# Kernel tuning notes

Hardware: AMD Instinct MI355X
Metric: run time of the kernel (lower is better)

Reference implementation:

```python
import jax, jax.numpy as jnp
import numpy as np

N, C, T, H, W = 16, 64, 30, 64, 44
PC = 64
OUT_H, OUT_W = 16, 20
T_RATE, H_RATE, W_RATE = 0.4, 4.0 / 8, 10.0 / 11  # torso
HEAD_H_RATE = 1.0 / 8
EPS = 1e-8


def setup_inputs() -> dict:
    key = jax.random.key(0)
    ks = jax.random.split(key, 8)
    x = jax.random.normal(ks[0], (N, C, T, H, W), jnp.float32)
    param_x = jax.random.normal(ks[1], (N, PC), jnp.float32)
    W1 = jax.random.normal(ks[2], (PC, PC // 2), jnp.float32) * 0.1
    b1 = jnp.zeros((PC // 2,), jnp.float32)
    W2 = jax.random.normal(ks[3], (PC // 2, 7), jnp.float32) * 0.1
    b2 = jnp.zeros((7,), jnp.float32)
    Wf = jax.random.normal(ks[4], (C, C), jnp.float32) * 0.05
    bf = jnp.zeros((C,), jnp.float32)
    return {"x": x, "param_x": param_x, "W1": W1, "b1": b1, "W2": W2, "b2": b2, "Wf": Wf, "bf": bf}


def reference(x, param_x, W1, b1, W2, b2, Wf, bf):
    n, c, t, h, w = x.shape
    dtype = x.dtype
    atten_in_t = t * T_RATE
    atten_in_h = h * H_RATE
    atten_in_w = w * W_RATE
    atten_ratio = atten_in_w / atten_in_h
    aout_h = int(round(OUT_W / atten_ratio))
    anchor_t = int(round(t / 2.0))
    anchor_x = int(round(w / 2.0))
    anchor_y = int(round(atten_in_h / 2.0 + h * HEAD_H_RATE))  # torso anchor

    # --- localization MLP (locator stand-in): param_x -> 7 params per sample ---
    hid = jnp.tanh(param_x @ W1 + b1)
    p = hid @ W2 + b2  # [N, 7]
    dt0, dx0, dy0 = p[:, 0:1], p[:, 1:2], p[:, 2:3]
    log_sigma2, log_delta_t, log_delta, log_gamma = p[:, 3:4], p[:, 4:5], p[:, 5:6], p[:, 6:7]

    dx = jnp.tanh(dx0) * atten_in_w / 2.0 + anchor_x          # [N,1]
    dy = jnp.tanh(dy0) * atten_in_h / 2.0 + anchor_y          # [N,1]
    sigma2 = jnp.exp(log_sigma2)                              # [N,1]
    delta = jnp.exp(log_delta) * W_RATE                      # [N,1]
    gamma = jax.nn.sigmoid(log_gamma)                         # [N,1]

    # --- spatial Gaussian filter banks ---
    gx = jnp.arange(OUT_W, dtype=dtype)
    gy = jnp.arange(aout_h, dtype=dtype)
    mu_x = dx + (gx - OUT_W / 2.0) * delta                    # [N, OUT_W]
    mu_y = dy + (gy - aout_h / 2.0) * delta                   # [N, aout_h]
    a = jnp.arange(w, dtype=dtype)
    b = jnp.arange(h, dtype=dtype)
    s2 = sigma2[:, :, None]                                   # [N,1,1]
    Fx = jnp.exp(-((a - mu_x[:, :, None]) ** 2) / (2.0 * s2))  # [N, OUT_W, W]
    Fy = jnp.exp(-((b - mu_y[:, :, None]) ** 2) / (2.0 * s2))  # [N, aout_h, H]
    Fx = Fx / jnp.maximum(jnp.sum(Fx, -1, keepdims=True), EPS)
    Fy = Fy / jnp.maximum(jnp.sum(Fy, -1, keepdims=True), EPS)

    # --- spatial sampling: Fy @ x @ Fx^T over the (C*T)-folded batch dim ---
    x2 = x.reshape(n, c * t, h, w)
    t1 = jnp.einsum('ndhw,nqw->ndhq', x2, Fx)                 # [N, C*T, H, OUT_W]
    g = jnp.einsum('nph,ndhq->ndpq', Fy, t1)                  # [N, C*T, aout_h, OUT_W]
    pad_t = (OUT_H - aout_h) // 2
    pad_b = OUT_H - pad_t - aout_h
    g = jnp.pad(g, ((0, 0), (0, 0), (pad_t, pad_b), (0, 0)))  # [N, C*T, OUT_H, OUT_W]

    # --- temporal linear resampling (grid_sample, align_corners=True, zero pad) ---
    dt = jnp.tanh(dt0) * atten_in_t / 2.0 + anchor_t          # [N,1]
    delta_t = jnp.exp(log_delta_t) * T_RATE                   # [N,1]
    gt = jnp.arange(t, dtype=dtype)
    mu_t = dt + (gt - t / 2.0) * delta_t                      # [N, T] raw frame positions

    gseq = g.reshape(n, c, t, OUT_H * OUT_W).transpose(0, 1, 3, 2).reshape(n, c * OUT_H * OUT_W, t)
    i0f = jnp.floor(mu_t)
    frac = mu_t - i0f
    i0 = i0f.astype(jnp.int32)
    i1 = i0 + 1

    def gather(idx):
        return jnp.take_along_axis(gseq, jnp.clip(idx, 0, t - 1)[:, None, :], axis=2)

    w0 = jnp.where((i0 >= 0) & (i0 < t), 1.0 - frac, 0.0)[:, None, :]
    w1 = jnp.where((i1 >= 0) & (i1 < t), frac, 0.0)[:, None, :]
    samp = gather(i0) * w0 + gather(i1) * w1                  # [N, C*OUT_H*OUT_W, T]
    out = samp.reshape(n, c, OUT_H, OUT_W, t).transpose(0, 1, 4, 2, 3)  # [N,C,T,OUT_H,OUT_W]

    out = out * gamma.reshape(n, 1, 1, 1, 1)
    # feature extraction: pointwise Conv3d (extractor stand-in)
    out = jnp.einsum('ncthw,oc->nothw', out, Wf) + bf[None, :, None, None, None]

    params = jnp.stack([dt[:, 0], dx[:, 0], dy[:, 0], sigma2[:, 0],
                        delta[:, 0], delta_t[:, 0], gamma[:, 0]], 0)  # [7, N]
    return out, jax.lax.stop_gradient(params)
```

## Files before the change

kernel.cpp:

```cpp
#include <hip/hip_runtime.h>
#include <math.h>

#define NN 16
#define CC 64
#define TT 30
#define HH 64
#define WW 44
#define OUTH 16
#define OUTW 20
#define HW 320

#define FX_OFF    0
#define FY_OFF    14080
#define IDX0_OFF  30464
#define IDX1_OFF  30944
#define TW0_OFF   31424
#define TW1_OFF   31904
#define GAM_OFF   32384
#define G_OFF     32400

__global__ __launch_bounds__(64) void params_kernel(
    const float* __restrict__ param_x, const float* __restrict__ W1,
    const float* __restrict__ b1, const float* __restrict__ W2,
    const float* __restrict__ b2, float* __restrict__ ws,
    float* __restrict__ params_out) {
  int n = blockIdx.x;
  int tid = threadIdx.x;
  __shared__ float px[64];
  __shared__ float hid[32];
  __shared__ float pv[7];

  px[tid] = param_x[n * 64 + tid];
  __syncthreads();
  if (tid < 32) {
    float s = b1[tid];
    #pragma unroll
    for (int k = 0; k < 64; ++k) s += px[k] * W1[k * 32 + tid];
    hid[tid] = tanhf(s);
  }
  __syncthreads();
  if (tid < 7) {
    float s = b2[tid];
    #pragma unroll
    for (int j = 0; j < 32; ++j) s += hid[j] * W2[j * 7 + tid];
    pv[tid] = s;
  }
  __syncthreads();

  float dt      = tanhf(pv[0]) * 6.0f  + 15.0f;
  float dx      = tanhf(pv[1]) * 20.0f + 22.0f;
  float dy      = tanhf(pv[2]) * 16.0f + 24.0f;
  float sigma2  = expf(pv[3]);
  float delta_t = expf(pv[4]) * 0.4f;
  float delta   = expf(pv[5]) * (10.0f / 11.0f);
  float gamma   = 1.0f / (1.0f + expf(-pv[6]));
  float inv2s2  = 1.0f / (2.0f * sigma2);

  if (tid < 20) {
    float mu = dx + ((float)tid - 10.0f) * delta;
    float vals[44];
    float s = 0.0f;
    #pragma unroll
    for (int w = 0; w < 44; ++w) {
      float d = (float)w - mu;
      float e = expf(-d * d * inv2s2);
      vals[w] = e; s += e;
    }
    float inv = 1.0f / fmaxf(s, 1e-8f);
    float* Fx = ws + FX_OFF + n * (20 * 44) + tid * 44;
    #pragma unroll
    for (int w = 0; w < 44; ++w) Fx[w] = vals[w] * inv;
  }
  if (tid < 16) {
    float mu = dy + ((float)tid - 8.0f) * delta;
    float vals[64];
    float s = 0.0f;
    #pragma unroll
    for (int h = 0; h < 64; ++h) {
      float d = (float)h - mu;
      float e = expf(-d * d * inv2s2);
      vals[h] = e; s += e;
    }
    float inv = 1.0f / fmaxf(s, 1e-8f);
    float* Fy = ws + FY_OFF + n * (16 * 64) + tid * 64;
    #pragma unroll
    for (int h = 0; h < 64; ++h) Fy[h] = vals[h] * inv;
  }
  if (tid < 30) {
    float mu = dt + ((float)tid - 15.0f) * delta_t;
    float i0f = floorf(mu);
    float frac = mu - i0f;
    int i0 = (int)i0f;
    int i1 = i0 + 1;
    float w0 = (i0 >= 0 && i0 < TT) ? (1.0f - frac) : 0.0f;
    float w1 = (i1 >= 0 && i1 < TT) ? frac : 0.0f;
    ((int*)(ws + IDX0_OFF))[n * TT + tid] = min(max(i0, 0), TT - 1);
    ((int*)(ws + IDX1_OFF))[n * TT + tid] = min(max(i1, 0), TT - 1);
    ws[TW0_OFF + n * TT + tid] = w0;
    ws[TW1_OFF + n * TT + tid] = w1;
  }
  if (tid == 0) {
    ws[GAM_OFF + n] = gamma;
    params_out[0 * NN + n] = dt;
    params_out[1 * NN + n] = dx;
    params_out[2 * NN + n] = dy;
    params_out[3 * NN + n] = sigma2;
    params_out[4 * NN + n] = delta;
    params_out[5 * NN + n] = delta_t;
    params_out[6 * NN + n] = gamma;
  }
}

__global__ __launch_bounds__(256) void spatial_kernel(
    const float* __restrict__ x, const float* __restrict__ fxbuf,
    const float* __restrict__ fybuf, float* __restrict__ g) {
  int b = blockIdx.x;
  int n  = b / (TT * 16);
  int r  = b % (TT * 16);
  int t  = r / 16;
  int c0 = (r % 16) * 4;

  int tid  = threadIdx.x;
  int cl   = tid >> 6;
  int lane = tid & 63;

  __shared__ float st1[4 * 20 * 68];
  __shared__ float sFy[16 * 68];

  {
    const float* Fy = fybuf + n * (16 * 64);
    #pragma unroll
    for (int i = tid; i < 16 * 64; i += 256) {
      int p = i >> 6, h = i & 63;
      sFy[p * 68 + h] = Fy[i];
    }
  }

  int c = c0 + cl;
  const float* xs = x + ((((size_t)n * CC + c) * TT + t) * HH + lane) * WW;
  float xrow[44];
  {
    const float4* xp = (const float4*)xs;
    #pragma unroll
    for (int i = 0; i < 11; ++i) {
      float4 v = xp[i];
      xrow[4 * i + 0] = v.x; xrow[4 * i + 1] = v.y;
      xrow[4 * i + 2] = v.z; xrow[4 * i + 3] = v.w;
    }
  }
  const float* fx = fxbuf + n * (20 * 44);
  float acc[20];
  #pragma unroll
  for (int q = 0; q < 20; ++q) {
    float s = 0.0f;
    #pragma unroll
    for (int w = 0; w < 44; ++w) s = fmaf(xrow[w], fx[q * 44 + w], s);
    acc[q] = s;
  }
  #pragma unroll
  for (int q = 0; q < 20; ++q) st1[(cl * 20 + q) * 68 + lane] = acc[q];
  __syncthreads();

  int p  = lane >> 2;
  int qg = lane & 3;
  float o[5] = {0.f, 0.f, 0.f, 0.f, 0.f};
  #pragma unroll
  for (int hc = 0; hc < 16; ++hc) {
    float4 fy = *(const float4*)&sFy[p * 68 + hc * 4];
    #pragma unroll
    for (int j = 0; j < 5; ++j) {
      int q = qg * 5 + j;
      float4 tv = *(const float4*)&st1[(cl * 20 + q) * 68 + hc * 4];
      o[j] = fmaf(fy.x, tv.x, fmaf(fy.y, tv.y, fmaf(fy.z, tv.z, fmaf(fy.w, tv.w, o[j]))));
    }
  }
  float* gout = g + ((size_t)((n * CC + c) * TT + t)) * HW + p * OUTW + qg * 5;
  #pragma unroll
  for (int j = 0; j < 5; ++j) gout[j] = o[j];
}

__global__ __launch_bounds__(256) void output_kernel(
    const float* __restrict__ g, const float* __restrict__ ws,
    const float* __restrict__ Wf, const float* __restrict__ bf,
    float* __restrict__ out) {
  int b = blockIdx.x;
  int n    = b / (TT * 2);
  int r    = b % (TT * 2);
  int tp   = r >> 1;
  int hw0  = (r & 1) * 160;
  int tid  = threadIdx.x;

  __shared__ float sWfT[64 * 65];
  __shared__ float smix[64 * 160];

  #pragma unroll
  for (int i = tid; i < 64 * 64; i += 256) {
    int oc = i >> 6, c = i & 63;
    sWfT[c * 65 + oc] = Wf[i];
  }

  int i0 = ((const int*)(ws + IDX0_OFF))[n * TT + tp];
  int i1 = ((const int*)(ws + IDX1_OFF))[n * TT + tp];
  float w0 = ws[TW0_OFF + n * TT + tp];
  float w1 = ws[TW1_OFF + n * TT + tp];
  float gamma = ws[GAM_OFF + n];

  #pragma unroll
  for (int i = tid; i < 64 * 160; i += 256) {
    int c = i / 160, hwl = i % 160;
    size_t base = (size_t)(n * CC + c) * TT;
    float g0 = g[(base + i0) * HW + hw0 + hwl];
    float g1 = g[(base + i1) * HW + hw0 + hwl];
    smix[i] = gamma * (w0 * g0 + w1 * g1);
  }
  __syncthreads();

  int ocg = tid >> 5;
  int hwg = tid & 31;
  int oc0 = ocg * 8;
  int hwl0 = hwg * 5;
  float acc[8][5];
  #pragma unroll
  for (int u = 0; u < 8; ++u)
    #pragma unroll
    for (int j = 0; j < 5; ++j) acc[u][j] = 0.0f;

  #pragma unroll 4
  for (int c = 0; c < 64; ++c) {
    float4 wv0 = *(const float4*)&sWfT[c * 65 + oc0];
    float4 wv1 = *(const float4*)&sWfT[c * 65 + oc0 + 4];
    float m[5];
    #pragma unroll
    for (int j = 0; j < 5; ++j) m[j] = smix[c * 160 + hwl0 + j];
    float wv[8] = {wv0.x, wv0.y, wv0.z, wv0.w, wv1.x, wv1.y, wv1.z, wv1.w};
    #pragma unroll
    for (int u = 0; u < 8; ++u)
      #pragma unroll
      for (int j = 0; j < 5; ++j) acc[u][j] = fmaf(wv[u], m[j], acc[u][j]);
  }

  #pragma unroll
  for (int u = 0; u < 8; ++u) {
    int oc = oc0 + u;
    float bias = bf[oc];
    float* op = out + (((size_t)n * CC + oc) * TT + tp) * HW + hw0 + hwl0;
    #pragma unroll
    for (int j = 0; j < 5; ++j) op[j] = acc[u][j] + bias;
  }
}

extern "C" void kernel_launch(void* const* d_in, const int* in_sizes, int n_in,
                              void* d_out, int out_size, void* d_ws,
                              size_t ws_size, hipStream_t stream) {
  const float* x       = (const float*)d_in[0];
  const float* param_x = (const float*)d_in[1];
  const float* W1      = (const float*)d_in[2];
  const float* b1      = (const float*)d_in[3];
  const float* W2      = (const float*)d_in[4];
  const float* b2      = (const float*)d_in[5];
  const float* Wf      = (const float*)d_in[6];
  const float* bf      = (const float*)d_in[7];
  float* out = (float*)d_out;
  float* ws  = (float*)d_ws;
  float* params_out = out + (size_t)NN * CC * TT * HW;

  params_kernel<<<NN, 64, 0, stream>>>(param_x, W1, b1, W2, b2, ws, params_out);
  spatial_kernel<<<NN * TT * 16, 256, 0, stream>>>(
      x, ws + FX_OFF, ws + FY_OFF, ws + G_OFF);
  output_kernel<<<NN * TT * 2, 256, 0, stream>>>(ws + G_OFF, ws, Wf, bf, out);
}
```

Before: 546.6 us.

## Skip x rows and columns outside the Gaussian filter support window

The params kernel now works out, per sample, a column and row window (rounded to multiples of 4) outside which the Gaussian filter weights fall below about exp(-30). The spatial kernel loads and contracts only x rows and float4 column chunks inside that window. Its second-stage contraction loops only over the active row range, splits that range between the two half-waves, and merges the halves with a cross-lane shuffle. The output kernel's temporal gather now uses float4 loads and stores. The window cuts memory traffic and FMAs on x, but it drops tiny tail contributions and adds control flow that depends on the data.

```diff
diff --git a/kernel.cpp b/kernel.cpp
--- a/kernel.cpp
+++ b/kernel.cpp
@@ -17,7 +17,8 @@
 #define TW0_OFF   31424
 #define TW1_OFF   31904
 #define GAM_OFF   32384
-#define G_OFF     32400
+#define RNG_OFF   32400
+#define G_OFF     32464
 
 __global__ __launch_bounds__(64) void params_kernel(
     const float* __restrict__ param_x, const float* __restrict__ W1,
@@ -100,6 +101,17 @@
     ws[TW1_OFF + n * TT + tid] = w1;
   }
   if (tid == 0) {
+    float R = 7.7459667f * sqrtf(sigma2);
+    int wlo = max(0,  (int)floorf(dx - 10.0f * delta - R));
+    int whi = min(43, (int)ceilf (dx +  9.0f * delta + R));
+    int hlo = max(0,  (int)floorf(dy -  8.0f * delta - R));
+    int hhi = min(63, (int)ceilf (dy +  7.0f * delta + R));
+    int* rng = (int*)(ws + RNG_OFF) + n * 4;
+    rng[0] = wlo & ~3;
+    rng[1] = whi | 3;
+    rng[2] = hlo & ~3;
+    rng[3] = hhi | 3;
+
     ws[GAM_OFF + n] = gamma;
     params_out[0 * NN + n] = dt;
     params_out[1 * NN + n] = dx;
@@ -112,8 +124,8 @@
 }
 
 __global__ __launch_bounds__(256) void spatial_kernel(
-    const float* __restrict__ x, const float* __restrict__ fxbuf,
-    const float* __restrict__ fybuf, float* __restrict__ g) {
+    const float* __restrict__ x, const float* __restrict__ ws,
+    float* __restrict__ g) {
   int b = blockIdx.x;
   int n  = b / (TT * 16);
   int r  = b % (TT * 16);
@@ -127,56 +139,81 @@
   __shared__ float st1[4 * 20 * 68];
   __shared__ float sFy[16 * 68];
 
+  const int* rng = (const int*)(ws + RNG_OFF) + n * 4;
+  int wlo4 = rng[0], whi4 = rng[1], hlo4 = rng[2], hhi4 = rng[3];
+
   {
-    const float* Fy = fybuf + n * (16 * 64);
-    #pragma unroll
-    for (int i = tid; i < 16 * 64; i += 256) {
-      int p = i >> 6, h = i & 63;
-      sFy[p * 68 + h] = Fy[i];
-    }
+    const float4* Fy4 = (const float4*)(ws + FY_OFF + n * (16 * 64));
+    float4 v = Fy4[tid];
+    int p = tid >> 4, h4 = tid & 15;
+    *(float4*)&sFy[p * 68 + h4 * 4] = v;
   }
 
   int c = c0 + cl;
-  const float* xs = x + ((((size_t)n * CC + c) * TT + t) * HH + lane) * WW;
-  float xrow[44];
-  {
-    const float4* xp = (const float4*)xs;
+  bool hact = (lane >= hlo4) && (lane <= hhi4);
+  if (hact) {
+    const float4* xp =
+        (const float4*)(x + ((((size_t)n * CC + c) * TT + t) * HH + lane) * WW);
+    int ilo = wlo4 >> 2, ihi = whi4 >> 2;
+    float xrow[44];
     #pragma unroll
     for (int i = 0; i < 11; ++i) {
-      float4 v = xp[i];
+      float4 v;
+      if (i >= ilo && i <= ihi) v = xp[i];
+      else v = make_float4(0.0f, 0.0f, 0.0f, 0.0f);
       xrow[4 * i + 0] = v.x; xrow[4 * i + 1] = v.y;
       xrow[4 * i + 2] = v.z; xrow[4 * i + 3] = v.w;
     }
-  }
-  const float* fx = fxbuf + n * (20 * 44);
-  float acc[20];
-  #pragma unroll
-  for (int q = 0; q < 20; ++q) {
-    float s = 0.0f;
-    #pragma unroll
-    for (int w = 0; w < 44; ++w) s = fmaf(xrow[w], fx[q * 44 + w], s);
-    acc[q] = s;
-  }
-  #pragma unroll
-  for (int q = 0; q < 20; ++q) st1[(cl * 20 + q) * 68 + lane] = acc[q];
-  __syncthreads();
-
-  int p  = lane >> 2;
+    const float* fx = ws + FX_OFF + n * (20 * 44);
+    #pragma unroll
+    for (int q = 0; q < 20; ++q) {
+      float s = 0.0f;
+      #pragma unroll
+      for (int w = 0; w < 44; ++w) s = fmaf(xrow[w], fx[q * 44 + w], s);
+      st1[(cl * 20 + q) * 68 + lane] = s;
+    }
+  }
+  __syncthreads();
+
+  int hh = lane >> 5;
+  int pp = (lane >> 2) & 7;
   int qg = lane & 3;
-  float o[5] = {0.f, 0.f, 0.f, 0.f, 0.f};
-  #pragma unroll
-  for (int hc = 0; hc < 16; ++hc) {
-    float4 fy = *(const float4*)&sFy[p * 68 + hc * 4];
+  int hc0 = hlo4 >> 2, hc1 = hhi4 >> 2;
+
+  float o[2][5];
+  #pragma unroll
+  for (int u = 0; u < 2; ++u)
+    #pragma unroll
+    for (int j = 0; j < 5; ++j) o[u][j] = 0.0f;
+
+  for (int hcc = hc0 + hh; hcc <= hc1; hcc += 2) {
+    float4 fy0 = *(const float4*)&sFy[pp * 68 + hcc * 4];
+    float4 fy1 = *(const float4*)&sFy[(pp + 8) * 68 + hcc * 4];
     #pragma unroll
     for (int j = 0; j < 5; ++j) {
       int q = qg * 5 + j;
-      float4 tv = *(const float4*)&st1[(cl * 20 + q) * 68 + hc * 4];
-      o[j] = fmaf(fy.x, tv.x, fmaf(fy.y, tv.y, fmaf(fy.z, tv.z, fmaf(fy.w, tv.w, o[j]))));
-    }
-  }
-  float* gout = g + ((size_t)((n * CC + c) * TT + t)) * HW + p * OUTW + qg * 5;
-  #pragma unroll
-  for (int j = 0; j < 5; ++j) gout[j] = o[j];
+      float4 tv = *(const float4*)&st1[(cl * 20 + q) * 68 + hcc * 4];
+      o[0][j] = fmaf(fy0.x, tv.x,
+                fmaf(fy0.y, tv.y, fmaf(fy0.z, tv.z, fmaf(fy0.w, tv.w, o[0][j]))));
+      o[1][j] = fmaf(fy1.x, tv.x,
+                fmaf(fy1.y, tv.y, fmaf(fy1.z, tv.z, fmaf(fy1.w, tv.w, o[1][j]))));
+    }
+  }
+  #pragma unroll
+  for (int u = 0; u < 2; ++u)
+    #pragma unroll
+    for (int j = 0; j < 5; ++j)
+      o[u][j] += __shfl_xor(o[u][j], 32);
+
+  if (hh == 0) {
+    float* gout = g + ((size_t)((n * CC + c) * TT + t)) * HW;
+    #pragma unroll
+    for (int u = 0; u < 2; ++u) {
+      int p = pp + u * 8;
+      #pragma unroll
+      for (int j = 0; j < 5; ++j) gout[p * OUTW + qg * 5 + j] = o[u][j];
+    }
+  }
 }
 
 __global__ __launch_bounds__(256) void output_kernel(
@@ -206,12 +243,18 @@
   float gamma = ws[GAM_OFF + n];
 
   #pragma unroll
-  for (int i = tid; i < 64 * 160; i += 256) {
-    int c = i / 160, hwl = i % 160;
+  for (int i4 = tid; i4 < 64 * 40; i4 += 256) {
+    int c  = i4 / 40;
+    int r4 = i4 - c * 40;
     size_t base = (size_t)(n * CC + c) * TT;
-    float g0 = g[(base + i0) * HW + hw0 + hwl];
-    float g1 = g[(base + i1) * HW + hw0 + hwl];
-    smix[i] = gamma * (w0 * g0 + w1 * g1);
+    float4 a  = *(const float4*)(g + (base + i0) * HW + hw0 + r4 * 4);
+    float4 bb = *(const float4*)(g + (base + i1) * HW + hw0 + r4 * 4);
+    float4 m;
+    m.x = gamma * fmaf(w0, a.x, w1 * bb.x);
+    m.y = gamma * fmaf(w0, a.y, w1 * bb.y);
+    m.z = gamma * fmaf(w0, a.z, w1 * bb.z);
+    m.w = gamma * fmaf(w0, a.w, w1 * bb.w);
+    *(float4*)&smix[c * 160 + r4 * 4] = m;
   }
   __syncthreads();
 
@@ -265,7 +308,6 @@
   float* params_out = out + (size_t)NN * CC * TT * HW;
 
   params_kernel<<<NN, 64, 0, stream>>>(param_x, W1, b1, W2, b2, ws, params_out);
-  spatial_kernel<<<NN * TT * 16, 256, 0, stream>>>(
-      x, ws + FX_OFF, ws + FY_OFF, ws + G_OFF);
+  spatial_kernel<<<NN * TT * 16, 256, 0, stream>>>(x, ws, ws + G_OFF);
   output_kernel<<<NN * TT * 2, 256, 0, stream>>>(ws + G_OFF, ws, Wf, bf, out);
 }
```

Result: faster. 508.9 us (-6.9%).
